# Optimization experiments

Measured on AMD Instinct MI355X. Metric: run time of the kernel, lower is better.

The kernel has to match this reference:

```python
import jax, jax.numpy as jnp
import numpy as np

N = 50000
E = 640000
H = 128
C = 3

def _xavier(key, shape, gain=1.0):
    fan_in, fan_out = shape[0], shape[1]
    a = gain * np.sqrt(6.0 / (fan_in + fan_out))
    return jax.random.uniform(key, shape, jnp.float32, -a, a)

def setup_inputs() -> dict:
    key = jax.random.key(0)
    ks = jax.random.split(key, 12)
    h = jax.random.normal(ks[0], (N, H), jnp.float32)
    x = jax.random.normal(ks[1], (N, C), jnp.float32)
    edge_index = jax.random.randint(ks[2], (2, E), 0, N, jnp.int64 if jax.config.jax_enable_x64 else jnp.int32)
    # edge_mlp: Linear(2H+1 -> H), SiLU, Linear(H -> H), SiLU
    We1 = _xavier(ks[3], (2 * H + 1, H)); be1 = jnp.zeros((H,), jnp.float32)
    We2 = _xavier(ks[4], (H, H));          be2 = jnp.zeros((H,), jnp.float32)
    # coord_mlp: Linear(H -> H), SiLU, Linear(H -> 1, no bias, gain 0.01)
    Wc1 = _xavier(ks[5], (H, H)); bc1 = jnp.zeros((H,), jnp.float32)
    Wc2 = _xavier(ks[6], (H, 1), gain=0.01)
    # node_mlp: Linear(2H -> H), SiLU, Linear(H -> H)
    Wn1 = _xavier(ks[7], (2 * H, H)); bn1 = jnp.zeros((H,), jnp.float32)
    Wn2 = _xavier(ks[8], (H, H));     bn2 = jnp.zeros((H,), jnp.float32)
    return dict(h=h, x=x, edge_index=edge_index,
                We1=We1, be1=be1, We2=We2, be2=be2,
                Wc1=Wc1, bc1=bc1, Wc2=Wc2,
                Wn1=Wn1, bn1=bn1, Wn2=Wn2, bn2=bn2)

def reference(h, x, edge_index, We1, be1, We2, be2, Wc1, bc1, Wc2, Wn1, bn1, Wn2, bn2):
    src, dst = edge_index[0], edge_index[1]
    n = h.shape[0]
    rel_pos = x[src] - x[dst]                              # [E, C]
    dist_sq = jnp.sum(rel_pos * rel_pos, axis=-1, keepdims=True)  # [E, 1]
    edge_input = jnp.concatenate([h[src], h[dst], dist_sq], axis=-1)  # [E, 2H+1]
    m_ij = jax.nn.silu(edge_input @ We1 + be1)
    m_ij = jax.nn.silu(m_ij @ We2 + be2)                   # [E, H]
    coord_weight = jax.nn.silu(m_ij @ Wc1 + bc1) @ Wc2     # [E, 1]
    coord_agg = jax.ops.segment_sum(rel_pos * coord_weight, dst, num_segments=n)
    x_out = x + coord_agg
    msg_agg = jax.ops.segment_sum(m_ij, dst, num_segments=n)  # [N, H]
    node_input = jnp.concatenate([h, msg_agg], axis=-1)    # [N, 2H]
    h_upd = jax.nn.silu(node_input @ Wn1 + bn1) @ Wn2 + bn2
    h_out = h + h_upd
    return (h_out, x_out)
```

## Files before the change

### kernel.cpp

```cpp
#include <hip/hip_runtime.h>

#define H 128

typedef __bf16 bf8_t __attribute__((ext_vector_type(8)));
typedef float  f4_t  __attribute__((ext_vector_type(4)));

#define MFMA16(a, b, c) __builtin_amdgcn_mfma_f32_16x16x32_bf16((a), (b), (c), 0, 0, 0)

__device__ __forceinline__ float silu_f(float v) {
    return v * (1.0f / (1.0f + __expf(-v)));
}

__device__ __forceinline__ void bar_lds() {
    asm volatile("s_waitcnt lgkmcnt(0)\ns_barrier" ::: "memory");
}

__device__ __forceinline__ float wload(const void* p, int idx, bool f32) {
    return f32 ? ((const float*)p)[idx] : (float)((const __bf16*)p)[idx];
}

__device__ __forceinline__ bf8_t hload8(const void* p, size_t off, bool f32) {
    bf8_t v;
    if (f32) {
        const float4* q = (const float4*)((const float*)p + off);
        const float4 a = q[0], b = q[1];
        v[0]=(__bf16)a.x; v[1]=(__bf16)a.y; v[2]=(__bf16)a.z; v[3]=(__bf16)a.w;
        v[4]=(__bf16)b.x; v[5]=(__bf16)b.y; v[6]=(__bf16)b.z; v[7]=(__bf16)b.w;
    } else {
        v = *(const bf8_t*)((const __bf16*)p + off);
    }
    return v;
}

__device__ __forceinline__ int eidx(const void* ei, int i, bool i64) {
    return i64 ? (int)((const long long*)ei)[i] : ((const int*)ei)[i];
}

__global__ void detect_kernel(const unsigned short* __restrict__ hraw,
                              const int* __restrict__ eiraw, int* __restrict__ flags)
{
    __shared__ int s_nf, s_oddnz;
    if (threadIdx.x == 0) { s_nf = 0; s_oddnz = 0; }
    __syncthreads();
    int nf = 0;
    for (int i = threadIdx.x; i < 16384; i += blockDim.x) {
        const unsigned short u = hraw[i];
        if (((u >> 7) & 0xFF) == 0xFF) nf++;
    }
    int onz = 0;
    for (int i = threadIdx.x; i < 512; i += blockDim.x) {
        if (eiraw[2*i + 1] != 0) onz++;
    }
    if (nf)  atomicAdd(&s_nf, nf);
    if (onz) atomicAdd(&s_oddnz, onz);
    __syncthreads();
    if (threadIdx.x == 0) {
        flags[0] = (s_nf > 0) ? 1 : 0;
        flags[1] = (s_oddnz == 0) ? 1 : 0;
    }
}

__global__ void histd_kernel(const void* __restrict__ ei, int* __restrict__ cnt,
                             const int* __restrict__ flags, int Ee)
{
    const int e = blockIdx.x*blockDim.x + threadIdx.x;
    if (e < Ee) atomicAdd(&cnt[eidx(ei, Ee + e, flags[1] != 0)], 1);
}

__global__ void scanA_kernel(const int* __restrict__ cnt, int* __restrict__ bsum, int Nn)
{
    __shared__ int s[512];
    const int gi = blockIdx.x*512 + threadIdx.x;
    s[threadIdx.x] = (gi < Nn) ? cnt[gi] : 0;
    __syncthreads();
    for (int off = 256; off > 0; off >>= 1) {
        if (threadIdx.x < off) s[threadIdx.x] += s[threadIdx.x + off];
        __syncthreads();
    }
    if (threadIdx.x == 0) bsum[blockIdx.x] = s[0];
}

__global__ void scanB_kernel(int* __restrict__ bsum, int* __restrict__ base, int nCh)
{
    if (threadIdx.x == 0) {
        int acc = 0;
        for (int b = 0; b < nCh; ++b) { base[b] = acc; acc += bsum[b]; }
    }
}

__global__ void scanC_kernel(const int* __restrict__ cnt, const int* __restrict__ base,
                             int* __restrict__ off, int* __restrict__ cursor, int Nn)
{
    __shared__ int s[512];
    const int i  = threadIdx.x;
    const int gi = blockIdx.x*512 + i;
    const int v  = (gi < Nn) ? cnt[gi] : 0;
    s[i] = v;
    __syncthreads();
    for (int o = 1; o < 512; o <<= 1) {
        const int t = (i >= o) ? s[i - o] : 0;
        __syncthreads();
        s[i] += t;
        __syncthreads();
    }
    const int excl = s[i] - v;
    if (gi <= Nn) {
        const int val = base[blockIdx.x] + excl;
        off[gi] = val;
        if (gi < Nn) cursor[gi] = val;
    }
}

__global__ void scatgeo_kernel(const void* __restrict__ ei, int* __restrict__ cursor,
                               int* __restrict__ srcs, int* __restrict__ dsts,
                               float* __restrict__ d2buf, float4* __restrict__ rel4,
                               const void* __restrict__ x,
                               const int* __restrict__ flags, int Ee)
{
    const int e = blockIdx.x*blockDim.x + threadIdx.x;
    if (e >= Ee) return;
    const bool i64 = flags[1] != 0;
    const bool f32 = flags[0] != 0;
    const int s = eidx(ei, e, i64);
    const int d = eidx(ei, Ee + e, i64);
    const int p = atomicAdd(&cursor[d], 1);
    srcs[p] = s;
    dsts[p] = d;
    float r[3];
    #pragma unroll
    for (int c = 0; c < 3; ++c)
        r[c] = wload(x, s*3 + c, f32) - wload(x, d*3 + c, f32);
    const float d2 = r[0]*r[0] + r[1]*r[1] + r[2]*r[2];
    d2buf[p] = d2;
    float4 o; o.x = r[0]; o.y = r[1]; o.z = r[2]; o.w = d2;
    rel4[p] = o;
}

__global__ __launch_bounds__(512, 2)
void proj_kernel(const void* __restrict__ h, const void* __restrict__ We1,
                 const void* __restrict__ be1, const int* __restrict__ flags,
                 __bf16* __restrict__ PB, int Nn)
{
    const bool f32 = flags[0] != 0;
    const int tid  = threadIdx.x;
    const int wv   = tid >> 6;
    const int lane = tid & 63;
    const int quad = lane >> 4;
    const int l15  = lane & 15;

    bf8_t bW[4][2];
    float bias[2];
    #pragma unroll
    for (int t = 0; t < 2; ++t) {
        const int n    = wv*32 + t*16 + l15;
        const int rb   = (n < 128) ? 0 : 128;
        const int col  = n & 127;
        #pragma unroll
        for (int kc = 0; kc < 4; ++kc) {
            bf8_t v;
            #pragma unroll
            for (int j = 0; j < 8; ++j)
                v[j] = (__bf16)wload(We1, (rb + kc*32 + quad*8 + j)*H + col, f32);
            bW[kc][t] = v;
        }
        bias[t] = (n < 128) ? 0.f : wload(be1, col, f32);
    }

    __shared__ __bf16 s_h[32*136];

    const int tiles = (Nn + 31) >> 5;
    for (int tile = blockIdx.x; tile < tiles; tile += gridDim.x) {
        const int nb = tile << 5;
        __syncthreads();
        {
            const int m = tid >> 4, c = tid & 15;
            int node = nb + m; if (node >= Nn) node = Nn - 1;
            *(bf8_t*)&s_h[m*136 + c*8] = hload8(h, (size_t)node*H + c*8, f32);
        }
        __syncthreads();

        f4_t acc[2][2];
        #pragma unroll
        for (int mm = 0; mm < 2; ++mm)
            #pragma unroll
            for (int t = 0; t < 2; ++t) acc[mm][t] = (f4_t){0.f,0.f,0.f,0.f};
        #pragma unroll
        for (int kc = 0; kc < 4; ++kc) {
            #pragma unroll
            for (int mm = 0; mm < 2; ++mm) {
                const bf8_t a = *(const bf8_t*)&s_h[(mm*16 + l15)*136 + quad*8 + kc*32];
                acc[mm][0] = MFMA16(a, bW[kc][0], acc[mm][0]);
                acc[mm][1] = MFMA16(a, bW[kc][1], acc[mm][1]);
            }
        }
        #pragma unroll
        for (int mm = 0; mm < 2; ++mm)
            #pragma unroll
            for (int i = 0; i < 4; ++i) {
                const int row = nb + mm*16 + quad*4 + i;
                if (row < Nn) {
                    #pragma unroll
                    for (int t = 0; t < 2; ++t)
                        PB[(size_t)row*256 + wv*32 + t*16 + l15] =
                            (__bf16)(acc[mm][t][i] + bias[t]);
                }
            }
    }
}

__global__ __launch_bounds__(512, 2)
void egnn_edge_pipe_kernel(const __bf16* __restrict__ PB,
                           const int* __restrict__ srcs, const int* __restrict__ dsts,
                           const float* __restrict__ d2buf,
                           const void* __restrict__ We1,
                           const void* __restrict__ We2, const void* __restrict__ be2,
                           const void* __restrict__ Wc1, const void* __restrict__ bc1,
                           const void* __restrict__ Wc2, const int* __restrict__ flags,
                           __bf16* __restrict__ m_buf, float* __restrict__ cw_buf,
                           int Ee)
{
    const bool f32 = flags[0] != 0;
    const int tid  = threadIdx.x;
    const int wv   = tid >> 6;
    const int lane = tid & 63;
    const int quad = lane >> 4;
    const int l15  = lane & 15;
    const int mg   = wv >> 2;
    const int ng   = wv & 3;

    bf8_t bW2[4][2], bWc[4][2];
    float be2v[2], bc1v[2], wc2v[2];
    #pragma unroll
    for (int t = 0; t < 2; ++t) {
        const int n = ng*32 + t*16 + l15;
        #pragma unroll
        for (int kc = 0; kc < 4; ++kc) {
            bf8_t v, u;
            #pragma unroll
            for (int j = 0; j < 8; ++j) {
                v[j] = (__bf16)wload(We2, (kc*32 + quad*8 + j)*H + n, f32);
                u[j] = (__bf16)wload(Wc1, (kc*32 + quad*8 + j)*H + n, f32);
            }
            bW2[kc][t] = v;
            bWc[kc][t] = u;
        }
        be2v[t] = wload(be2, n, f32);
        bc1v[t] = wload(bc1, n, f32);
        wc2v[t] = wload(Wc2, n, f32);
    }

    const int em = tid >> 3;
    const int ch = tid & 7;
    float w1dA[8], w1dB[8];
    #pragma unroll
    for (int j = 0; j < 8; ++j) {
        w1dA[j] = wload(We1, 256*H + ch*8 + j, f32);
        w1dB[j] = wload(We1, 256*H + (ch+8)*8 + j, f32);
    }

    __shared__ __bf16 s_m1[64*136];
    __shared__ __bf16 s_m2[64*136];
    __shared__ float  s_cw[64*4];

    const int tiles = (Ee + 63) >> 6;

    bf8_t rA0, rA1, rB0, rB1;
    float d2cur;
    int   s_n, d_n;
    float d2nxt;
    {
        int e0 = blockIdx.x*64 + em; if (e0 >= Ee) e0 = Ee - 1;
        const int sc = srcs[e0], dc = dsts[e0];
        d2cur = d2buf[e0];
        rA0 = *(const bf8_t*)(PB + (size_t)sc*256 + ch*8);
        rA1 = *(const bf8_t*)(PB + (size_t)sc*256 + (ch+8)*8);
        rB0 = *(const bf8_t*)(PB + (size_t)dc*256 + 128 + ch*8);
        rB1 = *(const bf8_t*)(PB + (size_t)dc*256 + 128 + (ch+8)*8);
        const int t1 = blockIdx.x + gridDim.x;
        const int tt = (t1 < tiles) ? t1 : blockIdx.x;
        int e1 = tt*64 + em; if (e1 >= Ee) e1 = Ee - 1;
        s_n = srcs[e1]; d_n = dsts[e1]; d2nxt = d2buf[e1];
    }

    for (int t = blockIdx.x; t < tiles; t += gridDim.x) {
        {
            bf8_t o0, o1;
            #pragma unroll
            for (int j = 0; j < 8; ++j) {
                const float f0 = (float)rA0[j] + (float)rB0[j] + d2cur*w1dA[j];
                const float f1 = (float)rA1[j] + (float)rB1[j] + d2cur*w1dB[j];
                o0[j] = (__bf16)silu_f(f0);
                o1[j] = (__bf16)silu_f(f1);
            }
            *(bf8_t*)&s_m1[em*136 + ch*8]       = o0;
            *(bf8_t*)&s_m1[em*136 + (ch+8)*8]   = o1;
        }
        {
            const int sc = s_n, dc = d_n;
            rA0 = *(const bf8_t*)(PB + (size_t)sc*256 + ch*8);
            rA1 = *(const bf8_t*)(PB + (size_t)sc*256 + (ch+8)*8);
            rB0 = *(const bf8_t*)(PB + (size_t)dc*256 + 128 + ch*8);
            rB1 = *(const bf8_t*)(PB + (size_t)dc*256 + 128 + (ch+8)*8);
            d2cur = d2nxt;
            const int t2 = t + 2*gridDim.x;
            const int tt = (t2 < tiles) ? t2 : t;
            int e2 = tt*64 + em; if (e2 >= Ee) e2 = Ee - 1;
            s_n = srcs[e2]; d_n = dsts[e2]; d2nxt = d2buf[e2];
        }
        bar_lds();

        {
            f4_t a2[2][2];
            #pragma unroll
            for (int mm = 0; mm < 2; ++mm)
                #pragma unroll
                for (int h2 = 0; h2 < 2; ++h2) a2[mm][h2] = (f4_t){0.f,0.f,0.f,0.f};
            #pragma unroll
            for (int kc = 0; kc < 4; ++kc) {
                #pragma unroll
                for (int mm = 0; mm < 2; ++mm) {
                    const bf8_t a = *(const bf8_t*)&s_m1[(mg*32 + mm*16 + l15)*136 + quad*8 + kc*32];
                    a2[mm][0] = MFMA16(a, bW2[kc][0], a2[mm][0]);
                    a2[mm][1] = MFMA16(a, bW2[kc][1], a2[mm][1]);
                }
            }
            #pragma unroll
            for (int mm = 0; mm < 2; ++mm)
                #pragma unroll
                for (int i = 0; i < 4; ++i) {
                    const int m = mg*32 + mm*16 + quad*4 + i;
                    s_m2[m*136 + ng*32 + l15]      = (__bf16)silu_f(a2[mm][0][i] + be2v[0]);
                    s_m2[m*136 + ng*32 + 16 + l15] = (__bf16)silu_f(a2[mm][1][i] + be2v[1]);
                }
        }
        bar_lds();

        {
            const int ms = tid >> 4, c2 = tid & 15;
            *(bf8_t*)(m_buf + ((size_t)t*64 + ms)*H + c2*8) =
                *(const bf8_t*)&s_m2[ms*136 + c2*8];
            *(bf8_t*)(m_buf + ((size_t)t*64 + 32 + ms)*H + c2*8) =
                *(const bf8_t*)&s_m2[(ms+32)*136 + c2*8];
        }

        {
            f4_t a3[2][2];
            #pragma unroll
            for (int mm = 0; mm < 2; ++mm)
                #pragma unroll
                for (int h2 = 0; h2 < 2; ++h2) a3[mm][h2] = (f4_t){0.f,0.f,0.f,0.f};
            #pragma unroll
            for (int kc = 0; kc < 4; ++kc) {
                #pragma unroll
                for (int mm = 0; mm < 2; ++mm) {
                    const bf8_t a = *(const bf8_t*)&s_m2[(mg*32 + mm*16 + l15)*136 + quad*8 + kc*32];
                    a3[mm][0] = MFMA16(a, bWc[kc][0], a3[mm][0]);
                    a3[mm][1] = MFMA16(a, bWc[kc][1], a3[mm][1]);
                }
            }
            float p[2][4];
            #pragma unroll
            for (int mm = 0; mm < 2; ++mm)
                #pragma unroll
                for (int i = 0; i < 4; ++i) {
                    const float v0 = silu_f(a3[mm][0][i] + bc1v[0]);
                    const float v1 = silu_f(a3[mm][1][i] + bc1v[1]);
                    p[mm][i] = v0*wc2v[0] + v1*wc2v[1];
                }
            #pragma unroll
            for (int off = 1; off < 16; off <<= 1)
                #pragma unroll
                for (int mm = 0; mm < 2; ++mm)
                    #pragma unroll
                    for (int i = 0; i < 4; ++i) p[mm][i] += __shfl_xor(p[mm][i], off, 64);
            if (l15 == 0) {
                #pragma unroll
                for (int mm = 0; mm < 2; ++mm)
                    #pragma unroll
                    for (int i = 0; i < 4; ++i)
                        s_cw[(mg*32 + mm*16 + quad*4 + i)*4 + ng] = p[mm][i];
            }
        }
        bar_lds();

        if (tid < 64)
            cw_buf[(size_t)t*64 + tid] =
                s_cw[tid*4] + s_cw[tid*4+1] + s_cw[tid*4+2] + s_cw[tid*4+3];
    }
}

__global__ __launch_bounds__(512)
void egnn_agg_kernel(const void* __restrict__ x, const int* __restrict__ off,
                     const __bf16* __restrict__ m_buf, const float* __restrict__ cw_buf,
                     const float4* __restrict__ rel4, __bf16* __restrict__ msgb,
                     const int* __restrict__ flags, void* __restrict__ out,
                     size_t obase, int Nn)
{
    const bool f32 = flags[0] != 0;
    const int wv = threadIdx.x >> 6, lane = threadIdx.x & 63;
    const int n = blockIdx.x*8 + wv;
    if (n >= Nn) return;
    const int p0 = off[n], p1 = off[n+1];

    float ms0 = 0.f, ms1 = 0.f, c0 = 0.f, c1 = 0.f, c2 = 0.f;
    const unsigned int* mb = (const unsigned int*)m_buf;
    for (int p = p0; p < p1; ++p) {
        const unsigned int u = mb[(size_t)p*64 + lane];
        ms0 += __uint_as_float(u << 16);
        ms1 += __uint_as_float(u & 0xffff0000u);
        const float cw = cw_buf[p];
        const float4 r = rel4[p];
        c0 += r.x*cw; c1 += r.y*cw; c2 += r.z*cw;
    }
    union { unsigned int u; __bf16 b[2]; } pk;
    pk.b[0] = (__bf16)ms0; pk.b[1] = (__bf16)ms1;
    *(unsigned int*)&msgb[(size_t)n*H + 2*lane] = pk.u;
    if (lane == 0) {
        float xd0, xd1, xd2;
        if (f32) { const float* xp = (const float*)x + (size_t)n*3; xd0=xp[0]; xd1=xp[1]; xd2=xp[2]; }
        else     { const __bf16* xp = (const __bf16*)x + (size_t)n*3; xd0=(float)xp[0]; xd1=(float)xp[1]; xd2=(float)xp[2]; }
        const float o0 = xd0 + c0, o1 = xd1 + c1, o2 = xd2 + c2;
        if (f32) {
            float* op = (float*)out + obase + (size_t)n*3;
            op[0] = o0; op[1] = o1; op[2] = o2;
        } else {
            __bf16* op = (__bf16*)out + obase + (size_t)n*3;
            op[0] = (__bf16)o0; op[1] = (__bf16)o1; op[2] = (__bf16)o2;
        }
    }
}

__global__ __launch_bounds__(512, 2)
void egnn_node_kernel(const void* __restrict__ h, const void* __restrict__ msg,
                      const void* __restrict__ Wn1, const void* __restrict__ bn1,
                      const void* __restrict__ Wn2, const void* __restrict__ bn2,
                      const int* __restrict__ flags, void* __restrict__ h_out,
                      int Nn, int msg_f32)
{
    const bool f32 = flags[0] != 0;
    const int tid  = threadIdx.x;
    const int wv   = tid >> 6;
    const int lane = tid & 63;
    const int quad = lane >> 4;
    const int l15  = lane & 15;
    const int mg   = wv >> 2;
    const int ng   = wv & 3;

    bf8_t bW1[8][2];
    bf8_t bW2[4][2];
    float b1v[2], b2v[2];
    #pragma unroll
    for (int t = 0; t < 2; ++t) {
        const int n = ng*32 + t*16 + l15;
        #pragma unroll
        for (int kc = 0; kc < 8; ++kc) {
            bf8_t v;
            #pragma unroll
            for (int j = 0; j < 8; ++j) v[j] = (__bf16)wload(Wn1, (kc*32 + quad*8 + j)*H + n, f32);
            bW1[kc][t] = v;
        }
        #pragma unroll
        for (int kc = 0; kc < 4; ++kc) {
            bf8_t v;
            #pragma unroll
            for (int j = 0; j < 8; ++j) v[j] = (__bf16)wload(Wn2, (kc*32 + quad*8 + j)*H + n, f32);
            bW2[kc][t] = v;
        }
        b1v[t] = wload(bn1, n, f32);
        b2v[t] = wload(bn2, n, f32);
    }

    __shared__ __bf16 s_in[32*264];
    __shared__ __bf16 s_t1[32*136];

    const int tiles = (Nn + 31) >> 5;
    for (int tile = blockIdx.x; tile < tiles; tile += gridDim.x) {
        const int nb = tile << 5;
        __syncthreads();
        #pragma unroll
        for (int r = 0; r < 2; ++r) {
            const int idx = tid + r*512;
            const int m = idx >> 5, c = idx & 31;
            int node = nb + m;
            if (node >= Nn) node = Nn - 1;
            if (c < 16) {
                *(bf8_t*)&s_in[m*264 + c*8] = hload8(h, (size_t)node*H + c*8, f32);
            } else if (msg_f32) {
                const float4* mp = (const float4*)((const float*)msg + (size_t)node*H + (c - 16)*8);
                const float4 v0 = mp[0], v1 = mp[1];
                __bf16* d = &s_in[m*264 + c*8];
                d[0] = (__bf16)v0.x; d[1] = (__bf16)v0.y; d[2] = (__bf16)v0.z; d[3] = (__bf16)v0.w;
                d[4] = (__bf16)v1.x; d[5] = (__bf16)v1.y; d[6] = (__bf16)v1.z; d[7] = (__bf16)v1.w;
            } else {
                *(bf8_t*)&s_in[m*264 + c*8] =
                    *(const bf8_t*)((const __bf16*)msg + (size_t)node*H + (c - 16)*8);
            }
        }
        __syncthreads();

        {
            f4_t a0 = {0.f,0.f,0.f,0.f}, a1 = {0.f,0.f,0.f,0.f};
            const int abase = (mg*16 + l15)*264 + quad*8;
            #pragma unroll
            for (int kc = 0; kc < 8; ++kc) {
                const bf8_t a = *(const bf8_t*)&s_in[abase + kc*32];
                a0 = MFMA16(a, bW1[kc][0], a0);
                a1 = MFMA16(a, bW1[kc][1], a1);
            }
            #pragma unroll
            for (int i = 0; i < 4; ++i) {
                const int m = mg*16 + quad*4 + i;
                s_t1[m*136 + ng*32 + l15]      = (__bf16)silu_f(a0[i] + b1v[0]);
                s_t1[m*136 + ng*32 + 16 + l15] = (__bf16)silu_f(a1[i] + b1v[1]);
            }
        }
        __syncthreads();

        {
            f4_t a0 = {0.f,0.f,0.f,0.f}, a1 = {0.f,0.f,0.f,0.f};
            const int abase = (mg*16 + l15)*136 + quad*8;
            #pragma unroll
            for (int kc = 0; kc < 4; ++kc) {
                const bf8_t a = *(const bf8_t*)&s_t1[abase + kc*32];
                a0 = MFMA16(a, bW2[kc][0], a0);
                a1 = MFMA16(a, bW2[kc][1], a1);
            }
            #pragma unroll
            for (int i = 0; i < 4; ++i) {
                const int node = nb + mg*16 + quad*4 + i;
                if (node < Nn) {
                    const int n0 = ng*32 + l15, n1 = n0 + 16;
                    const size_t i0 = (size_t)node*H + n0, i1 = (size_t)node*H + n1;
                    const float h0 = f32 ? ((const float*)h)[i0] : (float)((const __bf16*)h)[i0];
                    const float h1 = f32 ? ((const float*)h)[i1] : (float)((const __bf16*)h)[i1];
                    const float o0 = a0[i] + b2v[0] + h0;
                    const float o1 = a1[i] + b2v[1] + h1;
                    if (f32) {
                        ((float*)h_out)[i0] = o0;
                        ((float*)h_out)[i1] = o1;
                    } else {
                        ((__bf16*)h_out)[i0] = (__bf16)o0;
                        ((__bf16*)h_out)[i1] = (__bf16)o1;
                    }
                }
            }
        }
    }
}

__global__ void cvt_ei_kernel(const void* __restrict__ src, int* __restrict__ dst,
                              int n, const int* __restrict__ flags)
{
    const int i = blockIdx.x*blockDim.x + threadIdx.x;
    if (i >= n) return;
    dst[i] = flags[1] ? (int)((const long long*)src)[i] : ((const int*)src)[i];
}

__global__ __launch_bounds__(512, 2)
void egnn_edge_kernel(const void* __restrict__ h, const void* __restrict__ x,
                      const int* __restrict__ ei,
                      const void* __restrict__ We1, const void* __restrict__ be1,
                      const void* __restrict__ We2, const void* __restrict__ be2,
                      const void* __restrict__ Wc1, const void* __restrict__ bc1,
                      const void* __restrict__ Wc2, const int* __restrict__ flags,
                      float* __restrict__ msg_agg, float* __restrict__ coord_agg,
                      int Nn, int Ee)
{
    const bool f32 = flags[0] != 0;
    const int tid  = threadIdx.x;
    const int wv   = tid >> 6;
    const int lane = tid & 63;
    const int quad = lane >> 4;
    const int l15  = lane & 15;
    const int mg   = wv >> 2;
    const int ng   = wv & 3;

    bf8_t bW1[8][2];
    bf8_t bW2[4][2];
    bf8_t bWc[4][2];
    float be1v[2], be2v[2], bc1v[2], w1dv[2], wc2v[2];
    #pragma unroll
    for (int t = 0; t < 2; ++t) {
        const int n = ng*32 + t*16 + l15;
        #pragma unroll
        for (int kc = 0; kc < 8; ++kc) {
            bf8_t v;
            #pragma unroll
            for (int j = 0; j < 8; ++j) v[j] = (__bf16)wload(We1, (kc*32 + quad*8 + j)*H + n, f32);
            bW1[kc][t] = v;
        }
        #pragma unroll
        for (int kc = 0; kc < 4; ++kc) {
            bf8_t v, u;
            #pragma unroll
            for (int j = 0; j < 8; ++j) {
                v[j] = (__bf16)wload(We2, (kc*32 + quad*8 + j)*H + n, f32);
                u[j] = (__bf16)wload(Wc1, (kc*32 + quad*8 + j)*H + n, f32);
            }
            bW2[kc][t] = v;
            bWc[kc][t] = u;
        }
        be1v[t] = wload(be1, n, f32);
        be2v[t] = wload(be2, n, f32);
        bc1v[t] = wload(bc1, n, f32);
        w1dv[t] = wload(We1, 256*H + n, f32);
        wc2v[t] = wload(Wc2, n, f32);
    }

    __shared__ __bf16 s_in[32*264];
    __shared__ __bf16 s_m1[32*136];
    __shared__ __bf16 s_m2[32*136];
    __shared__ float  s_rel[32*3];
    __shared__ float  s_dist[32];
    __shared__ int    s_dstv[32];
    __shared__ float  s_cw[32*4];

    const int tiles = Ee >> 5;
    for (int tile = blockIdx.x; tile < tiles; tile += gridDim.x) {
        const int ebase = tile << 5;
        __syncthreads();

        if (tid < 32) {
            const int e  = ebase + tid;
            const int sn = ei[e];
            const int dn = ei[Ee + e];
            s_dstv[tid] = dn;
            float d2 = 0.f;
            #pragma unroll
            for (int c = 0; c < 3; ++c) {
                float r;
                if (f32) r = ((const float*)x)[sn*3 + c] - ((const float*)x)[dn*3 + c];
                else     r = (float)((const __bf16*)x)[sn*3 + c] - (float)((const __bf16*)x)[dn*3 + c];
                s_rel[tid*3 + c] = r;
                d2 += r*r;
            }
            s_dist[tid] = d2;
        }
        #pragma unroll
        for (int r = 0; r < 2; ++r) {
            const int idx = tid + r*512;
            const int m = idx >> 5, c = idx & 31;
            const int e = ebase + m;
            const int node = (c < 16) ? ei[e] : ei[Ee + e];
            *(bf8_t*)&s_in[m*264 + c*8] = hload8(h, (size_t)node*H + (c & 15)*8, f32);
        }
        __syncthreads();

        {
            f4_t a0 = {0.f,0.f,0.f,0.f}, a1 = {0.f,0.f,0.f,0.f};
            const int abase = (mg*16 + l15)*264 + quad*8;
            #pragma unroll
            for (int kc = 0; kc < 8; ++kc) {
                const bf8_t a = *(const bf8_t*)&s_in[abase + kc*32];
                a0 = MFMA16(a, bW1[kc][0], a0);
                a1 = MFMA16(a, bW1[kc][1], a1);
            }
            #pragma unroll
            for (int i = 0; i < 4; ++i) {
                const int m = mg*16 + quad*4 + i;
                const float d2 = s_dist[m];
                s_m1[m*136 + ng*32 + l15]      = (__bf16)silu_f(a0[i] + d2*w1dv[0] + be1v[0]);
                s_m1[m*136 + ng*32 + 16 + l15] = (__bf16)silu_f(a1[i] + d2*w1dv[1] + be1v[1]);
            }
        }
        __syncthreads();

        {
            f4_t a0 = {0.f,0.f,0.f,0.f}, a1 = {0.f,0.f,0.f,0.f};
            const int abase = (mg*16 + l15)*136 + quad*8;
            #pragma unroll
            for (int kc = 0; kc < 4; ++kc) {
                const bf8_t a = *(const bf8_t*)&s_m1[abase + kc*32];
                a0 = MFMA16(a, bW2[kc][0], a0);
                a1 = MFMA16(a, bW2[kc][1], a1);
            }
            #pragma unroll
            for (int i = 0; i < 4; ++i) {
                const int m = mg*16 + quad*4 + i;
                const float v0 = silu_f(a0[i] + be2v[0]);
                const float v1 = silu_f(a1[i] + be2v[1]);
                s_m2[m*136 + ng*32 + l15]      = (__bf16)v0;
                s_m2[m*136 + ng*32 + 16 + l15] = (__bf16)v1;
                const size_t db = (size_t)s_dstv[m]*H + ng*32 + l15;
                atomicAdd(&msg_agg[db],      v0);
                atomicAdd(&msg_agg[db + 16], v1);
            }
        }
        __syncthreads();

        {
            f4_t a0 = {0.f,0.f,0.f,0.f}, a1 = {0.f,0.f,0.f,0.f};
            const int abase = (mg*16 + l15)*136 + quad*8;
            #pragma unroll
            for (int kc = 0; kc < 4; ++kc) {
                const bf8_t a = *(const bf8_t*)&s_m2[abase + kc*32];
                a0 = MFMA16(a, bWc[kc][0], a0);
                a1 = MFMA16(a, bWc[kc][1], a1);
            }
            float p[4];
            #pragma unroll
            for (int i = 0; i < 4; ++i) {
                const float v0 = silu_f(a0[i] + bc1v[0]);
                const float v1 = silu_f(a1[i] + bc1v[1]);
                p[i] = v0*wc2v[0] + v1*wc2v[1];
            }
            #pragma unroll
            for (int off = 1; off < 16; off <<= 1) {
                #pragma unroll
                for (int i = 0; i < 4; ++i) p[i] += __shfl_xor(p[i], off, 64);
            }
            if (l15 == 0) {
                #pragma unroll
                for (int i = 0; i < 4; ++i)
                    s_cw[(mg*16 + quad*4 + i)*4 + ng] = p[i];
            }
        }
        __syncthreads();

        if (tid < 96) {
            const int m = tid / 3, c = tid - m*3;
            const float cw = s_cw[m*4 + 0] + s_cw[m*4 + 1] + s_cw[m*4 + 2] + s_cw[m*4 + 3];
            atomicAdd(&coord_agg[(size_t)s_dstv[m]*3 + c], s_rel[m*3 + c]*cw);
        }
    }
}

__global__ void egnn_x_kernel(const void* __restrict__ x, const float* __restrict__ coord_agg,
                              const int* __restrict__ flags, void* __restrict__ out,
                              size_t obase, int total)
{
    const bool f32 = flags[0] != 0;
    const int i = blockIdx.x*blockDim.x + threadIdx.x;
    if (i >= total) return;
    const float xv = f32 ? ((const float*)x)[i] : (float)((const __bf16*)x)[i];
    const float o = xv + coord_agg[i];
    if (f32) ((float*)out)[obase + i] = o;
    else     ((__bf16*)out)[obase + i] = (__bf16)o;
}

static inline size_t align256(size_t v) { return (v + 255) & ~(size_t)255; }

extern "C" void kernel_launch(void* const* d_in, const int* in_sizes, int n_in,
                              void* d_out, int out_size, void* d_ws, size_t ws_size,
                              hipStream_t stream)
{
    const void* h   = d_in[0];
    const void* x   = d_in[1];
    const void* ei0 = d_in[2];
    const void* We1 = d_in[3];
    const void* be1 = d_in[4];
    const void* We2 = d_in[5];
    const void* be2 = d_in[6];
    const void* Wc1 = d_in[7];
    const void* bc1 = d_in[8];
    const void* Wc2 = d_in[9];
    const void* Wn1 = d_in[10];
    const void* bn1 = d_in[11];
    const void* Wn2 = d_in[12];
    const void* bn2 = d_in[13];

    const int Nn = in_sizes[0] / H;
    const int Ee = in_sizes[2] / 2;
    const int EeP = ((Ee + 63) & ~63) + 64;

    char* ws = (char*)d_ws;
    size_t o = 0;
    size_t o_mbuf  = o; o = align256(o + (size_t)EeP*H*2);
    size_t o_msg   = o; o = align256(o + (size_t)Nn*H*2);
    size_t o_srcs  = o; o = align256(o + (size_t)Ee*4);
    size_t o_dsts  = o; o = align256(o + (size_t)Ee*4);
    size_t o_cw    = o; o = align256(o + (size_t)EeP*4);
    size_t o_d2    = o; o = align256(o + (size_t)Ee*4);
    size_t o_rel   = o; o = align256(o + (size_t)Ee*16);
    size_t o_pb    = o; o = align256(o + (size_t)Nn*256*2);
    size_t o_cnt   = o; o = align256(o + (size_t)Nn*4);
    size_t o_off   = o; o = align256(o + (size_t)(Nn+1)*4);
    size_t o_cur   = o; o = align256(o + (size_t)Nn*4);
    size_t o_bsum  = o; o = align256(o + 512*4);
    size_t o_base  = o; o = align256(o + 512*4);
    size_t o_flags = o; o = align256(o + 64);
    const size_t need_csr = o;

    const int nCh = (Nn + 1 + 511) / 512;

    if (ws_size >= need_csr) {
        __bf16* m_buf   = (__bf16*)(ws + o_mbuf);
        __bf16* msgb    = (__bf16*)(ws + o_msg);
        int*    srcs    = (int*)   (ws + o_srcs);
        int*    dsts    = (int*)   (ws + o_dsts);
        float*  cw_buf  = (float*) (ws + o_cw);
        float*  d2buf   = (float*) (ws + o_d2);
        float4* rel4    = (float4*)(ws + o_rel);
        __bf16* PB      = (__bf16*)(ws + o_pb);
        int*    cnt     = (int*)   (ws + o_cnt);
        int*    off     = (int*)   (ws + o_off);
        int*    cursor  = (int*)   (ws + o_cur);
        int*    bsum    = (int*)   (ws + o_bsum);
        int*    base    = (int*)   (ws + o_base);
        int*    flags   = (int*)   (ws + o_flags);

        detect_kernel<<<1, 256, 0, stream>>>((const unsigned short*)h, (const int*)ei0, flags);
        hipMemsetAsync(cnt, 0, (size_t)Nn*4, stream);
        histd_kernel<<<(Ee + 511)/512, 512, 0, stream>>>(ei0, cnt, flags, Ee);
        scanA_kernel<<<nCh, 512, 0, stream>>>(cnt, bsum, Nn);
        scanB_kernel<<<1, 64, 0, stream>>>(bsum, base, nCh);
        scanC_kernel<<<nCh, 512, 0, stream>>>(cnt, base, off, cursor, Nn);
        scatgeo_kernel<<<(Ee + 511)/512, 512, 0, stream>>>(ei0, cursor, srcs, dsts,
                                                           d2buf, rel4, x, flags, Ee);
        proj_kernel<<<1024, 512, 0, stream>>>(h, We1, be1, flags, PB, Nn);

        egnn_edge_pipe_kernel<<<1024, 512, 0, stream>>>(PB, srcs, dsts, d2buf,
                                                        We1, We2, be2, Wc1, bc1, Wc2,
                                                        flags, m_buf, cw_buf, Ee);

        egnn_agg_kernel<<<(Nn + 7)/8, 512, 0, stream>>>(x, off, m_buf, cw_buf, rel4,
                                                        msgb, flags, d_out, (size_t)Nn*H, Nn);
        egnn_node_kernel<<<1024, 512, 0, stream>>>(h, msgb, Wn1, bn1, Wn2, bn2,
                                                   flags, d_out, Nn, 0);
    } else {
        float* msg_agg   = (float*)ws;
        float* coord_agg = (float*)(ws + (size_t)Nn*H*4);
        int*   ei        = (int*)  (ws + (size_t)Nn*H*4 + (size_t)Nn*3*4);
        int*   flags     = (int*)  (ws + (size_t)Nn*H*4 + (size_t)Nn*3*4 + (size_t)2*Ee*4);

        detect_kernel<<<1, 256, 0, stream>>>((const unsigned short*)h, (const int*)ei0, flags);
        cvt_ei_kernel<<<(2*Ee + 255)/256, 256, 0, stream>>>(ei0, ei, 2*Ee, flags);
        hipMemsetAsync(msg_agg,   0, (size_t)Nn*H*4, stream);
        hipMemsetAsync(coord_agg, 0, (size_t)Nn*3*4, stream);
        egnn_edge_kernel<<<1024, 512, 0, stream>>>(h, x, ei, We1, be1, We2, be2,
                                                   Wc1, bc1, Wc2, flags,
                                                   msg_agg, coord_agg, Nn, Ee);
        egnn_node_kernel<<<512, 512, 0, stream>>>(h, msg_agg, Wn1, bn1, Wn2, bn2,
                                                  flags, d_out, Nn, 1);
        egnn_x_kernel<<<(Nn*3 + 255)/256, 256, 0, stream>>>(x, coord_agg, flags, d_out,
                                                            (size_t)Nn*H, Nn*3);
    }
}
```

Measured before the change: 752.1 us.

## Fuse segmented aggregation into edge kernel, drop per-edge message buffer

```diff
diff --git a/kernel.cpp b/kernel.cpp
--- a/kernel.cpp
+++ b/kernel.cpp
@@ -113,8 +113,7 @@
 
 __global__ void scatgeo_kernel(const void* __restrict__ ei, int* __restrict__ cursor,
                                int* __restrict__ srcs, int* __restrict__ dsts,
-                               float* __restrict__ d2buf, float4* __restrict__ rel4,
-                               const void* __restrict__ x,
+                               float4* __restrict__ rel4, const void* __restrict__ x,
                                const int* __restrict__ flags, int Ee)
 {
     const int e = blockIdx.x*blockDim.x + threadIdx.x;
@@ -130,9 +129,8 @@
     #pragma unroll
     for (int c = 0; c < 3; ++c)
         r[c] = wload(x, s*3 + c, f32) - wload(x, d*3 + c, f32);
-    const float d2 = r[0]*r[0] + r[1]*r[1] + r[2]*r[2];
-    d2buf[p] = d2;
-    float4 o; o.x = r[0]; o.y = r[1]; o.z = r[2]; o.w = d2;
+    float4 o; o.x = r[0]; o.y = r[1]; o.z = r[2];
+    o.w = r[0]*r[0] + r[1]*r[1] + r[2]*r[2];
     rel4[p] = o;
 }
 
@@ -211,12 +209,12 @@
 __global__ __launch_bounds__(512, 2)
 void egnn_edge_pipe_kernel(const __bf16* __restrict__ PB,
                            const int* __restrict__ srcs, const int* __restrict__ dsts,
-                           const float* __restrict__ d2buf,
+                           const float4* __restrict__ rel4,
                            const void* __restrict__ We1,
                            const void* __restrict__ We2, const void* __restrict__ be2,
                            const void* __restrict__ Wc1, const void* __restrict__ bc1,
                            const void* __restrict__ Wc2, const int* __restrict__ flags,
-                           __bf16* __restrict__ m_buf, float* __restrict__ cw_buf,
+                           float* __restrict__ msg, float* __restrict__ coord,
                            int Ee)
 {
     const bool f32 = flags[0] != 0;
@@ -258,20 +256,29 @@
         w1dB[j] = wload(We1, 256*H + (ch+8)*8 + j, f32);
     }
 
+    const int rcol = tid >> 2;
+    const int rg   = tid & 3;
+    const int qb   = lane & ~3;
+
     __shared__ __bf16 s_m1[64*136];
     __shared__ __bf16 s_m2[64*136];
-    __shared__ float  s_cw[64*4];
+    __shared__ float  s_cw[4*64];
+    __shared__ int    s_dst[2][64];
+    __shared__ float4 s_rl[2][64];
 
     const int tiles = (Ee + 63) >> 6;
+    const float* rw = (const float*)rel4;
 
     bf8_t rA0, rA1, rB0, rB1;
-    float d2cur;
-    int   s_n, d_n;
-    float d2nxt;
+    float d2cur, d2nxt;
+    int   s_n, d_n, d_c;
+    float4 r4c, r4n;
     {
         int e0 = blockIdx.x*64 + em; if (e0 >= Ee) e0 = Ee - 1;
         const int sc = srcs[e0], dc = dsts[e0];
-        d2cur = d2buf[e0];
+        d_c = dc;
+        d2cur = rw[(size_t)e0*4 + 3];
+        if (ch == 0) r4c = rel4[e0];
         rA0 = *(const bf8_t*)(PB + (size_t)sc*256 + ch*8);
         rA1 = *(const bf8_t*)(PB + (size_t)sc*256 + (ch+8)*8);
         rB0 = *(const bf8_t*)(PB + (size_t)dc*256 + 128 + ch*8);
@@ -279,10 +286,13 @@
         const int t1 = blockIdx.x + gridDim.x;
         const int tt = (t1 < tiles) ? t1 : blockIdx.x;
         int e1 = tt*64 + em; if (e1 >= Ee) e1 = Ee - 1;
-        s_n = srcs[e1]; d_n = dsts[e1]; d2nxt = d2buf[e1];
-    }
-
-    for (int t = blockIdx.x; t < tiles; t += gridDim.x) {
+        s_n = srcs[e1]; d_n = dsts[e1]; d2nxt = rw[(size_t)e1*4 + 3];
+        if (ch == 0) r4n = rel4[e1];
+    }
+
+    int li = 0;
+    for (int t = blockIdx.x; t < tiles; t += gridDim.x, ++li) {
+        const int sb = li & 1;
         {
             bf8_t o0, o1;
             #pragma unroll
@@ -294,18 +304,21 @@
             }
             *(bf8_t*)&s_m1[em*136 + ch*8]       = o0;
             *(bf8_t*)&s_m1[em*136 + (ch+8)*8]   = o1;
-        }
-        {
-            const int sc = s_n, dc = d_n;
+            if (ch == 0) { s_dst[sb][em] = d_c; s_rl[sb][em] = r4c; }
+        }
+        {
+            const int sc = s_n, dc2 = d_n;
             rA0 = *(const bf8_t*)(PB + (size_t)sc*256 + ch*8);
             rA1 = *(const bf8_t*)(PB + (size_t)sc*256 + (ch+8)*8);
-            rB0 = *(const bf8_t*)(PB + (size_t)dc*256 + 128 + ch*8);
-            rB1 = *(const bf8_t*)(PB + (size_t)dc*256 + 128 + (ch+8)*8);
-            d2cur = d2nxt;
+            rB0 = *(const bf8_t*)(PB + (size_t)dc2*256 + 128 + ch*8);
+            rB1 = *(const bf8_t*)(PB + (size_t)dc2*256 + 128 + (ch+8)*8);
+            d_c = d_n; d2cur = d2nxt;
+            if (ch == 0) r4c = r4n;
             const int t2 = t + 2*gridDim.x;
             const int tt = (t2 < tiles) ? t2 : t;
             int e2 = tt*64 + em; if (e2 >= Ee) e2 = Ee - 1;
-            s_n = srcs[e2]; d_n = dsts[e2]; d2nxt = d2buf[e2];
+            s_n = srcs[e2]; d_n = dsts[e2]; d2nxt = rw[(size_t)e2*4 + 3];
+            if (ch == 0) r4n = rel4[e2];
         }
         bar_lds();
 
@@ -336,14 +349,6 @@
         bar_lds();
 
         {
-            const int ms = tid >> 4, c2 = tid & 15;
-            *(bf8_t*)(m_buf + ((size_t)t*64 + ms)*H + c2*8) =
-                *(const bf8_t*)&s_m2[ms*136 + c2*8];
-            *(bf8_t*)(m_buf + ((size_t)t*64 + 32 + ms)*H + c2*8) =
-                *(const bf8_t*)&s_m2[(ms+32)*136 + c2*8];
-        }
-
-        {
             f4_t a3[2][2];
             #pragma unroll
             for (int mm = 0; mm < 2; ++mm)
@@ -378,64 +383,103 @@
                 for (int mm = 0; mm < 2; ++mm)
                     #pragma unroll
                     for (int i = 0; i < 4; ++i)
-                        s_cw[(mg*32 + mm*16 + quad*4 + i)*4 + ng] = p[mm][i];
+                        s_cw[ng*64 + (mg*32 + mm*16 + quad*4 + i)] = p[mm][i];
+            }
+        }
+
+        {
+            const int rbase = rg*16;
+            int   curd = s_dst[sb][rbase];
+            float acc  = 0.f;
+            float pre  = 0.f;
+            int   predone = 0;
+            #pragma unroll
+            for (int i = 0; i < 16; ++i) {
+                const int   d = s_dst[sb][rbase + i];
+                const float v = (float)s_m2[(rbase + i)*136 + rcol];
+                if (d != curd) {
+                    if (!predone) { pre = acc; predone = 1; }
+                    else          { msg[(size_t)curd*H + rcol] = acc; }
+                    curd = d; acc = v;
+                } else acc += v;
+            }
+            const float suf = acc;
+            const int   whf = !predone;
+            float preA[4], sufA[4]; int whA[4];
+            #pragma unroll
+            for (int gg = 0; gg < 4; ++gg) {
+                preA[gg] = __shfl(pre, qb + gg, 64);
+                sufA[gg] = __shfl(suf, qb + gg, 64);
+                whA[gg]  = __shfl(whf, qb + gg, 64);
+            }
+            if (rg == 0) {
+                int   curd2 = s_dst[sb][0];
+                float cur   = 0.f;
+                int   first = 1;
+                #pragma unroll
+                for (int gg = 0; gg < 4; ++gg) {
+                    const int F = s_dst[sb][gg*16];
+                    const int L = s_dst[sb][gg*16 + 15];
+                    if (F != curd2) {
+                        if (first) atomicAdd(&msg[(size_t)curd2*H + rcol], cur);
+                        else       msg[(size_t)curd2*H + rcol] = cur;
+                        first = 0; curd2 = F; cur = 0.f;
+                    }
+                    if (whA[gg]) {
+                        cur += sufA[gg];
+                    } else {
+                        cur += preA[gg];
+                        if (first) atomicAdd(&msg[(size_t)curd2*H + rcol], cur);
+                        else       msg[(size_t)curd2*H + rcol] = cur;
+                        first = 0; curd2 = L; cur = sufA[gg];
+                    }
+                }
+                atomicAdd(&msg[(size_t)curd2*H + rcol], cur);
             }
         }
         bar_lds();
 
-        if (tid < 64)
-            cw_buf[(size_t)t*64 + tid] =
-                s_cw[tid*4] + s_cw[tid*4+1] + s_cw[tid*4+2] + s_cw[tid*4+3];
-    }
-}
-
-__global__ __launch_bounds__(512)
-void egnn_agg_kernel(const void* __restrict__ x, const int* __restrict__ off,
-                     const __bf16* __restrict__ m_buf, const float* __restrict__ cw_buf,
-                     const float4* __restrict__ rel4, __bf16* __restrict__ msgb,
-                     const int* __restrict__ flags, void* __restrict__ out,
-                     size_t obase, int Nn)
-{
-    const bool f32 = flags[0] != 0;
-    const int wv = threadIdx.x >> 6, lane = threadIdx.x & 63;
-    const int n = blockIdx.x*8 + wv;
-    if (n >= Nn) return;
-    const int p0 = off[n], p1 = off[n+1];
-
-    float ms0 = 0.f, ms1 = 0.f, c0 = 0.f, c1 = 0.f, c2 = 0.f;
-    const unsigned int* mb = (const unsigned int*)m_buf;
-    for (int p = p0; p < p1; ++p) {
-        const unsigned int u = mb[(size_t)p*64 + lane];
-        ms0 += __uint_as_float(u << 16);
-        ms1 += __uint_as_float(u & 0xffff0000u);
-        const float cw = cw_buf[p];
-        const float4 r = rel4[p];
-        c0 += r.x*cw; c1 += r.y*cw; c2 += r.z*cw;
-    }
-    union { unsigned int u; __bf16 b[2]; } pk;
-    pk.b[0] = (__bf16)ms0; pk.b[1] = (__bf16)ms1;
-    *(unsigned int*)&msgb[(size_t)n*H + 2*lane] = pk.u;
-    if (lane == 0) {
-        float xd0, xd1, xd2;
-        if (f32) { const float* xp = (const float*)x + (size_t)n*3; xd0=xp[0]; xd1=xp[1]; xd2=xp[2]; }
-        else     { const __bf16* xp = (const __bf16*)x + (size_t)n*3; xd0=(float)xp[0]; xd1=(float)xp[1]; xd2=(float)xp[2]; }
-        const float o0 = xd0 + c0, o1 = xd1 + c1, o2 = xd2 + c2;
-        if (f32) {
-            float* op = (float*)out + obase + (size_t)n*3;
-            op[0] = o0; op[1] = o1; op[2] = o2;
-        } else {
-            __bf16* op = (__bf16*)out + obase + (size_t)n*3;
-            op[0] = (__bf16)o0; op[1] = (__bf16)o1; op[2] = (__bf16)o2;
+        if (tid < 64) {
+            const int e = tid;
+            const float cwv = s_cw[e] + s_cw[64 + e] + s_cw[128 + e] + s_cw[192 + e];
+            const float4 r = s_rl[sb][e];
+            const int d = s_dst[sb][e];
+            float vx = r.x*cwv, vy = r.y*cwv, vz = r.z*cwv;
+            int   cn = 1;
+            #pragma unroll
+            for (int k = 1; k < 64; k <<= 1) {
+                const int   dk = __shfl_up(d,  k, 64);
+                const float xk = __shfl_up(vx, k, 64);
+                const float yk = __shfl_up(vy, k, 64);
+                const float zk = __shfl_up(vz, k, 64);
+                const int   ck = __shfl_up(cn, k, 64);
+                if (e >= k && dk == d) { vx += xk; vy += yk; vz += zk; cn += ck; }
+            }
+            const int dnx = __shfl_down(d, 1, 64);
+            const bool runend = (e == 63) || (dnx != d);
+            if (runend) {
+                const int rs = e - cn + 1;
+                if (rs == 0 || e == 63) {
+                    atomicAdd(&coord[(size_t)d*3 + 0], vx);
+                    atomicAdd(&coord[(size_t)d*3 + 1], vy);
+                    atomicAdd(&coord[(size_t)d*3 + 2], vz);
+                } else {
+                    coord[(size_t)d*3 + 0] = vx;
+                    coord[(size_t)d*3 + 1] = vy;
+                    coord[(size_t)d*3 + 2] = vz;
+                }
+            }
         }
     }
 }
 
 __global__ __launch_bounds__(512, 2)
-void egnn_node_kernel(const void* __restrict__ h, const void* __restrict__ msg,
+void egnn_node_kernel(const void* __restrict__ h, const float* __restrict__ msg,
                       const void* __restrict__ Wn1, const void* __restrict__ bn1,
                       const void* __restrict__ Wn2, const void* __restrict__ bn2,
                       const int* __restrict__ flags, void* __restrict__ h_out,
-                      int Nn, int msg_f32)
+                      const void* __restrict__ x, const float* __restrict__ coord,
+                      size_t obase, int do_x, int Nn)
 {
     const bool f32 = flags[0] != 0;
     const int tid  = threadIdx.x;
@@ -485,15 +529,22 @@
             if (node >= Nn) node = Nn - 1;
             if (c < 16) {
                 *(bf8_t*)&s_in[m*264 + c*8] = hload8(h, (size_t)node*H + c*8, f32);
-            } else if (msg_f32) {
-                const float4* mp = (const float4*)((const float*)msg + (size_t)node*H + (c - 16)*8);
+            } else {
+                const float4* mp = (const float4*)(msg + (size_t)node*H + (c - 16)*8);
                 const float4 v0 = mp[0], v1 = mp[1];
                 __bf16* d = &s_in[m*264 + c*8];
                 d[0] = (__bf16)v0.x; d[1] = (__bf16)v0.y; d[2] = (__bf16)v0.z; d[3] = (__bf16)v0.w;
                 d[4] = (__bf16)v1.x; d[5] = (__bf16)v1.y; d[6] = (__bf16)v1.z; d[7] = (__bf16)v1.w;
-            } else {
-                *(bf8_t*)&s_in[m*264 + c*8] =
-                    *(const bf8_t*)((const __bf16*)msg + (size_t)node*H + (c - 16)*8);
+            }
+        }
+        if (do_x && tid < 96) {
+            const int m = tid / 3, c = tid - m*3;
+            const int node = nb + m;
+            if (node < Nn) {
+                const float xv = wload(x, node*3 + c, f32);
+                const float o = xv + coord[(size_t)node*3 + c];
+                if (f32) ((float*)h_out)[obase + (size_t)node*3 + c] = o;
+                else     ((__bf16*)h_out)[obase + (size_t)node*3 + c] = (__bf16)o;
             }
         }
         __syncthreads();
@@ -761,19 +812,17 @@
 
     const int Nn = in_sizes[0] / H;
     const int Ee = in_sizes[2] / 2;
-    const int EeP = ((Ee + 63) & ~63) + 64;
 
     char* ws = (char*)d_ws;
     size_t o = 0;
-    size_t o_mbuf  = o; o = align256(o + (size_t)EeP*H*2);
-    size_t o_msg   = o; o = align256(o + (size_t)Nn*H*2);
+    size_t o_cnt   = o; o = align256(o + (size_t)Nn*4);
+    size_t o_msg   = o; o = align256(o + (size_t)Nn*H*4);
+    size_t o_coord = o; o = align256(o + (size_t)Nn*3*4);
+    const size_t zero_end = o;
     size_t o_srcs  = o; o = align256(o + (size_t)Ee*4);
     size_t o_dsts  = o; o = align256(o + (size_t)Ee*4);
-    size_t o_cw    = o; o = align256(o + (size_t)EeP*4);
-    size_t o_d2    = o; o = align256(o + (size_t)Ee*4);
     size_t o_rel   = o; o = align256(o + (size_t)Ee*16);
     size_t o_pb    = o; o = align256(o + (size_t)Nn*256*2);
-    size_t o_cnt   = o; o = align256(o + (size_t)Nn*4);
     size_t o_off   = o; o = align256(o + (size_t)(Nn+1)*4);
     size_t o_cur   = o; o = align256(o + (size_t)Nn*4);
     size_t o_bsum  = o; o = align256(o + 512*4);
@@ -784,15 +833,13 @@
     const int nCh = (Nn + 1 + 511) / 512;
 
     if (ws_size >= need_csr) {
-        __bf16* m_buf   = (__bf16*)(ws + o_mbuf);
-        __bf16* msgb    = (__bf16*)(ws + o_msg);
+        int*    cnt     = (int*)   (ws + o_cnt);
+        float*  msg     = (float*) (ws + o_msg);
+        float*  coord   = (float*) (ws + o_coord);
         int*    srcs    = (int*)   (ws + o_srcs);
         int*    dsts    = (int*)   (ws + o_dsts);
-        float*  cw_buf  = (float*) (ws + o_cw);
-        float*  d2buf   = (float*) (ws + o_d2);
         float4* rel4    = (float4*)(ws + o_rel);
         __bf16* PB      = (__bf16*)(ws + o_pb);
-        int*    cnt     = (int*)   (ws + o_cnt);
         int*    off     = (int*)   (ws + o_off);
         int*    cursor  = (int*)   (ws + o_cur);
         int*    bsum    = (int*)   (ws + o_bsum);
@@ -800,23 +847,22 @@
         int*    flags   = (int*)   (ws + o_flags);
 
         detect_kernel<<<1, 256, 0, stream>>>((const unsigned short*)h, (const int*)ei0, flags);
-        hipMemsetAsync(cnt, 0, (size_t)Nn*4, stream);
+        hipMemsetAsync(ws + o_cnt, 0, zero_end - o_cnt, stream);
         histd_kernel<<<(Ee + 511)/512, 512, 0, stream>>>(ei0, cnt, flags, Ee);
         scanA_kernel<<<nCh, 512, 0, stream>>>(cnt, bsum, Nn);
         scanB_kernel<<<1, 64, 0, stream>>>(bsum, base, nCh);
         scanC_kernel<<<nCh, 512, 0, stream>>>(cnt, base, off, cursor, Nn);
         scatgeo_kernel<<<(Ee + 511)/512, 512, 0, stream>>>(ei0, cursor, srcs, dsts,
-                                                           d2buf, rel4, x, flags, Ee);
-        proj_kernel<<<1024, 512, 0, stream>>>(h, We1, be1, flags, PB, Nn);
-
-        egnn_edge_pipe_kernel<<<1024, 512, 0, stream>>>(PB, srcs, dsts, d2buf,
-                                                        We1, We2, be2, Wc1, bc1, Wc2,
-                                                        flags, m_buf, cw_buf, Ee);
-
-        egnn_agg_kernel<<<(Nn + 7)/8, 512, 0, stream>>>(x, off, m_buf, cw_buf, rel4,
-                                                        msgb, flags, d_out, (size_t)Nn*H, Nn);
-        egnn_node_kernel<<<1024, 512, 0, stream>>>(h, msgb, Wn1, bn1, Wn2, bn2,
-                                                   flags, d_out, Nn, 0);
+                                                           rel4, x, flags, Ee);
+        proj_kernel<<<512, 512, 0, stream>>>(h, We1, be1, flags, PB, Nn);
+
+        egnn_edge_pipe_kernel<<<512, 512, 0, stream>>>(PB, srcs, dsts, rel4,
+                                                       We1, We2, be2, Wc1, bc1, Wc2,
+                                                       flags, msg, coord, Ee);
+
+        egnn_node_kernel<<<1024, 512, 0, stream>>>(h, msg, Wn1, bn1, Wn2, bn2,
+                                                   flags, d_out, x, coord,
+                                                   (size_t)Nn*H, 1, Nn);
     } else {
         float* msg_agg   = (float*)ws;
         float* coord_agg = (float*)(ws + (size_t)Nn*H*4);
@@ -831,7 +877,8 @@
                                                    Wc1, bc1, Wc2, flags,
                                                    msg_agg, coord_agg, Nn, Ee);
         egnn_node_kernel<<<512, 512, 0, stream>>>(h, msg_agg, Wn1, bn1, Wn2, bn2,
-                                                  flags, d_out, Nn, 1);
+                                                  flags, d_out, x, coord_agg,
+                                                  (size_t)Nn*H, 0, Nn);
         egnn_x_kernel<<<(Nn*3 + 255)/256, 256, 0, stream>>>(x, coord_agg, flags, d_out,
                                                             (size_t)Nn*H, Nn*3);
     }
```

Result: faster. 673.1 us (-10.5%).
